# Kernel optimization log

Hardware: AMD Instinct MI355X
Metric: run time of the kernel (lower is better)

The kernel has to match this reference:

```python
import jax, jax.numpy as jnp
import numpy as np

HEADS = 8
EPS = 1e-5


def setup_inputs() -> dict:
    key = jax.random.key(0)
    ks = jax.random.split(key, 8)
    B, S, C = 2, 1024, 640
    n_refs = 4
    return {
        "hidden_states": jax.random.normal(ks[0], (B, S, C), jnp.float32),
        "ref_key": jax.random.normal(ks[1], (B, n_refs, S, C), jnp.float32),
        "ref_value": jax.random.normal(ks[2], (B, n_refs, S, C), jnp.float32),
        "Wq": jax.random.normal(ks[3], (C, C), jnp.float32) * (C ** -0.5),
        "Wk": jax.random.normal(ks[4], (C, C), jnp.float32) * (C ** -0.5),
        "Wv": jax.random.normal(ks[5], (C, C), jnp.float32) * (C ** -0.5),
        "Wo": jax.random.normal(ks[6], (C, C), jnp.float32) * (C ** -0.5),
        "bo": jnp.zeros((C,), jnp.float32),
    }


def reference(hidden_states, ref_key, ref_value, Wq, Wk, Wv, Wo, bo):
    B, S, C = hidden_states.shape
    H = HEADS
    D = C // H
    n = ref_key.shape[1]

    # projections (self-attention: encoder_hidden_states is None)
    q = hidden_states @ Wq
    k = hidden_states @ Wk
    v = hidden_states @ Wv

    def split_heads(x):  # [B, S, C] -> [B, H, S, D]
        return x.reshape(B, -1, H, D).transpose(0, 2, 1, 3)

    qh, kh, vh = split_heads(q), split_heads(k), split_heads(v)

    # per-reference head split: [B, n, S, C] -> [B, H, n, S, D]
    rk = ref_key.reshape(B, n, S, H, D).transpose(0, 3, 1, 2, 4)
    rv = ref_value.reshape(B, n, S, H, D).transpose(0, 3, 1, 2, 4)

    # AdaIN: style stats from value over its seq dim (unbiased std, as torch),
    # content stats per reference over that ref's seq dim.
    style_mean = vh.mean(axis=2, keepdims=True)[:, :, None]                 # [B,H,1,1,D]
    style_std = vh.std(axis=2, keepdims=True, ddof=1)[:, :, None] + EPS     # [B,H,1,1,D]
    content_mean = rv.mean(axis=3, keepdims=True)                           # [B,H,n,1,D]
    content_std = rv.std(axis=3, keepdims=True, ddof=1) + EPS               # [B,H,n,1,D]
    rv = (rv - content_mean) / content_std * style_std + style_mean

    # train_input=True: self KV first, then refs concatenated along kv axis
    k_ext = jnp.concatenate([kh, rk.reshape(B, H, n * S, D)], axis=2)  # [B,H,(1+n)S,D]
    v_ext = jnp.concatenate([vh, rv.reshape(B, H, n * S, D)], axis=2)

    scale = jnp.asarray(D, qh.dtype) ** -0.5
    scores = jnp.einsum("bhqd,bhkd->bhqk", qh, k_ext) * scale
    probs = jax.nn.softmax(scores, axis=-1)
    out = jnp.einsum("bhqk,bhkd->bhqd", probs, v_ext)

    out = out.transpose(0, 2, 1, 3).reshape(B, S, C)  # batch_to_head_dim
    return out @ Wo + bo  # to_out[0]; dropout is identity at eval
```

## Files before the change

kernel.cpp:

```cpp
#include <hip/hip_runtime.h>
#include <hip/hip_bf16.h>

typedef short short8 __attribute__((ext_vector_type(8)));
typedef short short4v __attribute__((ext_vector_type(4)));
typedef float f32x4 __attribute__((ext_vector_type(4)));

#define NB 2
#define NS 1024
#define NC 640
#define NH 8
#define ND 80
#define NRF 4
#define NL 5120
#define EPSF 1e-5f
#define QSCL 0.16129861f

__device__ __forceinline__ unsigned short f2bf(float f){
  unsigned int u = __float_as_uint(f);
  u += 0x7FFFu + ((u>>16)&1u);
  return (unsigned short)(u>>16);
}
__device__ __forceinline__ float bf2f(unsigned short s){
  return __uint_as_float(((unsigned)s)<<16);
}

__global__ void __launch_bounds__(256) k_cast_hs(const float* __restrict__ hs,
                                                 unsigned short* __restrict__ X){
  int i = (blockIdx.x*256 + threadIdx.x)*4;
  const float4 v = *(const float4*)(hs + i);
  uint2 pk;
  pk.x = (unsigned)f2bf(v.x) | ((unsigned)f2bf(v.y)<<16);
  pk.y = (unsigned)f2bf(v.z) | ((unsigned)f2bf(v.w)<<16);
  *(uint2*)(X + i) = pk;
}

__global__ void __launch_bounds__(256) k_transpose_w(const float* __restrict__ Wq,
    const float* __restrict__ Wk, const float* __restrict__ Wv, const float* __restrict__ Wo,
    unsigned short* __restrict__ WT){
  const float* W = (blockIdx.z==0)?Wq:(blockIdx.z==1)?Wk:(blockIdx.z==2)?Wv:Wo;
  unsigned short* out = WT + (size_t)blockIdx.z*NC*NC;
  int n0 = blockIdx.x*64, k0 = blockIdx.y*64;
  __shared__ unsigned short tile[64][65];
  int t = threadIdx.x;
  int cl = (t&15)*4, rl = t>>4;
  #pragma unroll
  for(int kk=0;kk<4;kk++){
    int kl = rl + kk*16;
    float4 v = *(const float4*)(W + (size_t)(k0+kl)*NC + n0 + cl);
    tile[kl][cl+0]=f2bf(v.x); tile[kl][cl+1]=f2bf(v.y);
    tile[kl][cl+2]=f2bf(v.z); tile[kl][cl+3]=f2bf(v.w);
  }
  __syncthreads();
  #pragma unroll
  for(int nn=0;nn<4;nn++){
    int nl = rl + nn*16;
    unsigned short a=tile[cl+0][nl], b=tile[cl+1][nl], c=tile[cl+2][nl], d=tile[cl+3][nl];
    uint2 pk; pk.x = (unsigned)a|((unsigned)b<<16); pk.y = (unsigned)c|((unsigned)d<<16);
    *(uint2*)(out + (size_t)(n0+nl)*NC + k0 + cl) = pk;
  }
}

__global__ void __launch_bounds__(256) k_gemm_qkv(const unsigned short* __restrict__ X,
    const unsigned short* __restrict__ WT, unsigned short* __restrict__ qbuf,
    unsigned short* __restrict__ kext, unsigned short* __restrict__ vTx){
  __shared__ unsigned short As[64*40], Bs[64*40];
  int mode = blockIdx.z;
  const unsigned short* Wt = WT + (size_t)mode*NC*NC;
  int M0 = blockIdx.x*64, N0 = blockIdx.y*64;
  int t = threadIdx.x, w = t>>6, lane = t&63, lr = lane&15, lg = lane>>4;
  int row = t>>2, seg = t&3;
  f32x4 acc[4];
  #pragma unroll
  for(int j=0;j<4;j++) acc[j] = (f32x4){0.f,0.f,0.f,0.f};
  for(int k0=0;k0<NC;k0+=32){
    uint4 a  = *(const uint4*)(X  + (size_t)(M0+row)*NC + k0 + seg*8);
    uint4 bq = *(const uint4*)(Wt + (size_t)(N0+row)*NC + k0 + seg*8);
    __syncthreads();
    *(uint4*)&As[row*40+seg*8] = a;
    *(uint4*)&Bs[row*40+seg*8] = bq;
    __syncthreads();
    short8 af = *(const short8*)&As[(w*16+lr)*40 + lg*8];
    #pragma unroll
    for(int j=0;j<4;j++){
      short8 bf = *(const short8*)&Bs[(j*16+lr)*40 + lg*8];
      acc[j] = __builtin_amdgcn_mfma_f32_16x16x32_bf16(af, bf, acc[j], 0,0,0);
    }
  }
  #pragma unroll
  for(int j=0;j<4;j++){
    int n = N0 + j*16 + lr;
    int h = n/ND, d = n - h*ND;
    #pragma unroll
    for(int r=0;r<4;r++){
      int m = M0 + w*16 + lg*4 + r;
      int b = m>>10, s = m&1023;
      float val = acc[j][r];
      if(mode==0){
        qbuf[(size_t)(((b<<3)|h)*NS + s)*ND + d] = f2bf(val*QSCL);
      } else if(mode==1){
        kext[(size_t)(((b<<3)|h)*NL + s)*ND + d] = f2bf(val);
      } else {
        vTx[(size_t)(((b<<3)|h)*ND + d)*NL + s] = f2bf(val);
      }
    }
  }
}

__global__ void __launch_bounds__(256) k_stats_self(const unsigned short* __restrict__ vTx,
    float* __restrict__ smean, float* __restrict__ sstd){
  int gw = blockIdx.x*4 + (threadIdx.x>>6);
  int lane = threadIdx.x&63;
  int b = gw/NC, c = gw%NC;
  int h = c/ND, d = c - h*ND;
  const unsigned short* row = vTx + (size_t)((b*NH + h)*ND + d)*NL;
  short8 v0 = *(const short8*)(row + lane*16);
  short8 v1 = *(const short8*)(row + lane*16 + 8);
  float sum=0.f, ss=0.f;
  #pragma unroll
  for(int j=0;j<8;j++){
    float x = bf2f((unsigned short)v0[j]); sum+=x; ss+=x*x;
    float y = bf2f((unsigned short)v1[j]); sum+=y; ss+=y*y;
  }
  #pragma unroll
  for(int m=1;m<=32;m<<=1){
    sum += __shfl_xor(sum, m);
    ss  += __shfl_xor(ss, m);
  }
  if(lane==0){
    float mean = sum*(1.f/1024.f);
    float var  = fmaxf(0.f,(ss - sum*sum*(1.f/1024.f))*(1.f/1023.f));
    smean[b*NC+c]=mean; sstd[b*NC+c]=sqrtf(var)+EPSF;
  }
}

__global__ void __launch_bounds__(256) k_stats_ref(const float* __restrict__ ref_value,
    float* __restrict__ cmean, float* __restrict__ cstd){
  int bid = blockIdx.x;
  int cg = bid%10, src = (bid/10)&3, b = bid/40;
  int t = threadIdx.x, cl = t&63, sg = t>>6;
  int c = cg*64 + cl;
  const float* base = ref_value + (size_t)(b*NRF + src)*NS*NC + c;
  float sum=0.f, ss=0.f;
  for(int i=0;i<256;i++){
    float x = base[(size_t)(sg*256+i)*NC];
    sum += x; ss += x*x;
  }
  __shared__ float r0[4][64], r1[4][64];
  r0[sg][cl]=sum; r1[sg][cl]=ss;
  __syncthreads();
  if(t<64){
    float S=0.f,Q=0.f;
    #pragma unroll
    for(int gg=0;gg<4;gg++){S+=r0[gg][t];Q+=r1[gg][t];}
    float mean = S*(1.f/1024.f);
    float var  = fmaxf(0.f,(Q - S*S*(1.f/1024.f))*(1.f/1023.f));
    int cc = cg*64+t;
    cmean[(b*NRF+src)*NC+cc]=mean;
    cstd[(b*NRF+src)*NC+cc]=sqrtf(var)+EPSF;
  }
}

__global__ void __launch_bounds__(256) k_scalebias(const float* __restrict__ smean,
    const float* __restrict__ sstd, const float* __restrict__ cmean, const float* __restrict__ cstd,
    float* __restrict__ scl, float* __restrict__ bia){
  int g = blockIdx.x*256+threadIdx.x;
  int c = g%NC; int b = g/(NRF*NC);
  float sc = sstd[b*NC+c]/cstd[g];
  bia[g] = smean[b*NC+c] - cmean[g]*sc;
  scl[g] = sc;
}

__global__ void __launch_bounds__(256) k_pack_k(const float* __restrict__ ref_key,
                                                unsigned short* __restrict__ kext){
  int g = blockIdx.x*256+threadIdx.x;
  size_t e = (size_t)g*4;
  int c = (int)(e%NC); int s = (int)((e/NC)&1023); int r = (int)((e/(NC*NS))&3); int b = (int)(e/((size_t)NC*NS*NRF));
  float4 v = *(const float4*)(ref_key + e);
  int h = c/ND, d = c - h*ND;
  uint2 pk;
  pk.x = (unsigned)f2bf(v.x)|((unsigned)f2bf(v.y)<<16);
  pk.y = (unsigned)f2bf(v.z)|((unsigned)f2bf(v.w)<<16);
  *(uint2*)(kext + (size_t)(((b<<3)|h)*NL + NS + r*NS + s)*ND + d) = pk;
}

__global__ void __launch_bounds__(256) k_pack_v(const float* __restrict__ ref_value,
    const float* __restrict__ scl, const float* __restrict__ bia, unsigned short* __restrict__ vTx){
  int bid=blockIdx.x;
  int ct=bid%10, st=(bid/10)&15, r=(bid/160)&3, b=bid/640;
  int c0=ct*64, s0=st*64;
  __shared__ float tile[64][68];
  int t=threadIdx.x;
  int cl=(t&15)*4, rl=t>>4;
  #pragma unroll
  for(int ss=0;ss<4;ss++){
    int srow = rl+ss*16;
    float4 v = *(const float4*)(ref_value + (size_t)((b*NRF+r)*NS + s0+srow)*NC + c0+cl);
    tile[srow][cl+0]=v.x; tile[srow][cl+1]=v.y; tile[srow][cl+2]=v.z; tile[srow][cl+3]=v.w;
  }
  __syncthreads();
  #pragma unroll
  for(int cc=0;cc<4;cc++){
    int crow = rl+cc*16;
    int c = c0+crow;
    float sc = scl[(b*NRF+r)*NC+c], bi = bia[(b*NRF+r)*NC+c];
    int h=c/ND, d=c-h*ND;
    unsigned short o0=f2bf(tile[(t&15)*4+0][crow]*sc+bi);
    unsigned short o1=f2bf(tile[(t&15)*4+1][crow]*sc+bi);
    unsigned short o2=f2bf(tile[(t&15)*4+2][crow]*sc+bi);
    unsigned short o3=f2bf(tile[(t&15)*4+3][crow]*sc+bi);
    uint2 pk; pk.x=(unsigned)o0|((unsigned)o1<<16); pk.y=(unsigned)o2|((unsigned)o3<<16);
    *(uint2*)(vTx + (size_t)(((b<<3)|h)*ND + d)*NL + NS + r*NS + s0 + (t&15)*4) = pk;
  }
}

__global__ void __launch_bounds__(256) k_attn(const unsigned short* __restrict__ qbuf,
    const unsigned short* __restrict__ kext, const unsigned short* __restrict__ vTx,
    float* __restrict__ pacc0, float* __restrict__ pacc1, float* __restrict__ pml){
  __shared__ unsigned short Ks[64*88];
  __shared__ unsigned short Vs[80*88];

  int p = blockIdx.x;
  int logical = (p&7)*64 + (p>>3);
  int tile = logical>>1;
  int part = logical&1;
  int bh = tile>>4, qti = tile&15;
  int t = threadIdx.x, w = t>>6, lane = t&63, lr = lane&15, lg = lane>>4;

  const unsigned short* kb = kext + (size_t)bh*NL*ND;
  const unsigned short* vb = vTx  + (size_t)bh*ND*NL;

  const unsigned short* qrow = qbuf + (size_t)(bh*NS + qti*64 + w*16 + lr)*ND;
  short8 qf0 = *(const short8*)(qrow + lg*8);
  short8 qf1 = *(const short8*)(qrow + 32 + lg*8);
  short4v q4 = *(const short4v*)(qrow + 64 + lg*4);
  short8 qft = {q4[0],q4[1],q4[2],q4[3],(short)0,(short)0,(short)0,(short)0};

  int rowA = t/10,       segA = t - 10*(t/10);
  int rowB = (t+256)/10, segB = (t+256) - 10*((t+256)/10);
  int rowC = (t+512)/10, segC = (t+512) - 10*((t+512)/10);
  int vd = t>>3, vs = t&7;

  f32x4 acc[5];
  #pragma unroll
  for(int dt=0;dt<5;dt++) acc[dt] = (f32x4){0.f,0.f,0.f,0.f};
  float mrun = -1e30f, lrun = 0.f;

  for(int i=0;i<40;i++){
    int key0 = (part*40 + i)*64;
    uint4 ra  = *(const uint4*)(kb + (size_t)(key0+rowA)*ND + segA*8);
    uint4 rb  = *(const uint4*)(kb + (size_t)(key0+rowB)*ND + segB*8);
    uint4 rc; if(t<128) rc = *(const uint4*)(kb + (size_t)(key0+rowC)*ND + segC*8);
    uint4 rv0 = *(const uint4*)(vb + (size_t)vd*NL + key0 + vs*8);
    uint4 rv1 = *(const uint4*)(vb + (size_t)(vd+32)*NL + key0 + vs*8);
    uint4 rv2; if(t<128) rv2 = *(const uint4*)(vb + (size_t)(vd+64)*NL + key0 + vs*8);
    __syncthreads();
    *(uint4*)&Ks[rowA*88 + segA*8] = ra;
    *(uint4*)&Ks[rowB*88 + segB*8] = rb;
    if(t<128) *(uint4*)&Ks[rowC*88 + segC*8] = rc;
    *(uint4*)&Vs[vd*88 + vs*8] = rv0;
    *(uint4*)&Vs[(vd+32)*88 + vs*8] = rv1;
    if(t<128) *(uint4*)&Vs[(vd+64)*88 + vs*8] = rv2;
    __syncthreads();

    f32x4 sc[4];
    #pragma unroll
    for(int mt=0;mt<4;mt++){
      const unsigned short* kr = &Ks[(mt*16+lr)*88];
      short8 kf0 = *(const short8*)(kr + lg*8);
      short8 kf1 = *(const short8*)(kr + 32 + lg*8);
      short4v k4 = *(const short4v*)(kr + 64 + lg*4);
      short8 kft = {k4[0],k4[1],k4[2],k4[3],(short)0,(short)0,(short)0,(short)0};
      f32x4 s = (f32x4){0.f,0.f,0.f,0.f};
      s = __builtin_amdgcn_mfma_f32_16x16x32_bf16(kf0, qf0, s, 0,0,0);
      s = __builtin_amdgcn_mfma_f32_16x16x32_bf16(kf1, qf1, s, 0,0,0);
      s = __builtin_amdgcn_mfma_f32_16x16x32_bf16(kft, qft, s, 0,0,0);
      sc[mt] = s;
    }

    float tmax = -1e30f;
    #pragma unroll
    for(int mt=0;mt<4;mt++){
      #pragma unroll
      for(int r=0;r<4;r++) tmax = fmaxf(tmax, sc[mt][r]);
    }
    tmax = fmaxf(tmax, __shfl_xor(tmax,16));
    tmax = fmaxf(tmax, __shfl_xor(tmax,32));
    float mnew = fmaxf(mrun, tmax);
    float corr = exp2f(mrun - mnew);
    float pvv[16]; float ps = 0.f;
    #pragma unroll
    for(int mt=0;mt<4;mt++){
      #pragma unroll
      for(int r=0;r<4;r++){ float e = exp2f(sc[mt][r]-mnew); pvv[mt*4+r]=e; ps+=e; }
    }
    ps += __shfl_xor(ps,16);
    ps += __shfl_xor(ps,32);
    lrun = lrun*corr + ps;
    mrun = mnew;
    #pragma unroll
    for(int dt=0;dt<5;dt++) acc[dt] *= corr;

    short8 pb[2];
    #pragma unroll
    for(int u=0;u<2;u++){
      #pragma unroll
      for(int j=0;j<4;j++){
        pb[u][j]   = (short)f2bf(pvv[u*8+j]);
        pb[u][4+j] = (short)f2bf(pvv[u*8+4+j]);
      }
    }
    #pragma unroll
    for(int u=0;u<2;u++){
      #pragma unroll
      for(int dt=0;dt<5;dt++){
        const unsigned short* vr = &Vs[(dt*16+lr)*88 + u*32 + lg*4];
        short4v v0 = *(const short4v*)(vr);
        short4v v1 = *(const short4v*)(vr + 16);
        short8 vf = {v0[0],v0[1],v0[2],v0[3],v1[0],v1[1],v1[2],v1[3]};
        acc[dt] = __builtin_amdgcn_mfma_f32_16x16x32_bf16(vf, pb[u], acc[dt], 0,0,0);
      }
    }
  }

  float* pa = (part ? pacc1 : pacc0) + (size_t)tile*5120;
  int q = w*16 + lr;
  #pragma unroll
  for(int dt=0;dt<5;dt++){
    *(f32x4*)(pa + q*80 + dt*16 + lg*4) = acc[dt];
  }
  if(lg==0){
    pml[(size_t)logical*128 + q*2 + 0] = mrun;
    pml[(size_t)logical*128 + q*2 + 1] = lrun;
  }
}

__global__ void __launch_bounds__(256) k_combine(const float* __restrict__ pacc0,
    const float* __restrict__ pacc1, const float* __restrict__ pml,
    unsigned short* __restrict__ attnO){
  int tile = blockIdx.x;
  int bh = tile>>4, qti = tile&15;
  int b = bh>>3, h = bh&7;
  int t = threadIdx.x;
  #pragma unroll
  for(int j=0;j<5;j++){
    int e = (t + j*256)*4;
    int q = e/80, d = e - (e/80)*80;
    float m0 = pml[(size_t)(tile*2+0)*128 + q*2], l0 = pml[(size_t)(tile*2+0)*128 + q*2 + 1];
    float m1 = pml[(size_t)(tile*2+1)*128 + q*2], l1 = pml[(size_t)(tile*2+1)*128 + q*2 + 1];
    float mm = fmaxf(m0,m1);
    float c0 = exp2f(m0-mm), c1 = exp2f(m1-mm);
    float inv = 1.f/(l0*c0 + l1*c1);
    c0 *= inv; c1 *= inv;
    float4 a0 = *(const float4*)(pacc0 + (size_t)tile*5120 + e);
    float4 a1 = *(const float4*)(pacc1 + (size_t)tile*5120 + e);
    uint2 pk;
    pk.x = (unsigned)f2bf(a0.x*c0+a1.x*c1) | ((unsigned)f2bf(a0.y*c0+a1.y*c1)<<16);
    pk.y = (unsigned)f2bf(a0.z*c0+a1.z*c1) | ((unsigned)f2bf(a0.w*c0+a1.w*c1)<<16);
    *(uint2*)(attnO + (size_t)(b*NS + qti*64 + q)*NC + h*ND + d) = pk;
  }
}

__global__ void __launch_bounds__(256) k_gemm_out(const unsigned short* __restrict__ A,
    const unsigned short* __restrict__ WT, const float* __restrict__ bo, float* __restrict__ out){
  __shared__ unsigned short As[64*40], Bs[64*40];
  const unsigned short* Wt = WT + (size_t)3*NC*NC;
  int M0 = blockIdx.x*64, N0 = blockIdx.y*64;
  int t = threadIdx.x, w = t>>6, lane = t&63, lr = lane&15, lg = lane>>4;
  int row = t>>2, seg = t&3;
  f32x4 acc[4];
  #pragma unroll
  for(int j=0;j<4;j++) acc[j] = (f32x4){0.f,0.f,0.f,0.f};
  for(int k0=0;k0<NC;k0+=32){
    uint4 a  = *(const uint4*)(A  + (size_t)(M0+row)*NC + k0 + seg*8);
    uint4 bq = *(const uint4*)(Wt + (size_t)(N0+row)*NC + k0 + seg*8);
    __syncthreads();
    *(uint4*)&As[row*40+seg*8] = a;
    *(uint4*)&Bs[row*40+seg*8] = bq;
    __syncthreads();
    short8 af = *(const short8*)&As[(w*16+lr)*40 + lg*8];
    #pragma unroll
    for(int j=0;j<4;j++){
      short8 bf = *(const short8*)&Bs[(j*16+lr)*40 + lg*8];
      acc[j] = __builtin_amdgcn_mfma_f32_16x16x32_bf16(af, bf, acc[j], 0,0,0);
    }
  }
  #pragma unroll
  for(int j=0;j<4;j++){
    int n = N0 + j*16 + lr;
    float bb = bo[n];
    #pragma unroll
    for(int r=0;r<4;r++){
      int m = M0 + w*16 + lg*4 + r;
      out[(size_t)m*NC + n] = acc[j][r] + bb;
    }
  }
}

extern "C" void kernel_launch(void* const* d_in, const int* in_sizes, int n_in,
                              void* d_out, int out_size, void* d_ws, size_t ws_size,
                              hipStream_t stream) {
  const float* hs        = (const float*)d_in[0];
  const float* ref_key   = (const float*)d_in[1];
  const float* ref_value = (const float*)d_in[2];
  const float* Wq = (const float*)d_in[3];
  const float* Wk = (const float*)d_in[4];
  const float* Wv = (const float*)d_in[5];
  const float* Wo = (const float*)d_in[6];
  const float* bo = (const float*)d_in[7];
  float* out = (float*)d_out;

  char* ws = (char*)d_ws;
  size_t off = 0;
  auto alloc = [&](size_t bytes)->char*{
    char* p = ws + off;
    off += (bytes + 255) & ~(size_t)255;
    return p;
  };
  unsigned short* X    = (unsigned short*)alloc((size_t)NB*NS*NC*2);
  unsigned short* WT   = (unsigned short*)alloc((size_t)4*NC*NC*2);
  unsigned short* qbuf = (unsigned short*)alloc((size_t)NB*NH*NS*ND*2);
  unsigned short* kext = (unsigned short*)alloc((size_t)NB*NH*NL*ND*2);
  unsigned short* vTx  = (unsigned short*)alloc((size_t)NB*NH*ND*NL*2);
  float* pacc1 = (float*)alloc((size_t)256*5120*4);
  float* pml   = (float*)alloc((size_t)512*128*4);
  float* smean = (float*)alloc((size_t)NB*NC*4);
  float* sstd  = (float*)alloc((size_t)NB*NC*4);
  float* cmean = (float*)alloc((size_t)NB*NRF*NC*4);
  float* cstd  = (float*)alloc((size_t)NB*NRF*NC*4);
  float* scl   = (float*)alloc((size_t)NB*NRF*NC*4);
  float* bia   = (float*)alloc((size_t)NB*NRF*NC*4);
  unsigned short* attn = X;
  float* pacc0 = out;

  k_cast_hs<<<1280, 256, 0, stream>>>(hs, X);
  k_transpose_w<<<dim3(10,10,4), 256, 0, stream>>>(Wq, Wk, Wv, Wo, WT);
  k_gemm_qkv<<<dim3(32,10,3), 256, 0, stream>>>(X, WT, qbuf, kext, vTx);
  k_pack_k<<<5120, 256, 0, stream>>>(ref_key, kext);
  k_stats_self<<<320, 256, 0, stream>>>(vTx, smean, sstd);
  k_stats_ref<<<80, 256, 0, stream>>>(ref_value, cmean, cstd);
  k_scalebias<<<20, 256, 0, stream>>>(smean, sstd, cmean, cstd, scl, bia);
  k_pack_v<<<1280, 256, 0, stream>>>(ref_value, scl, bia, vTx);
  k_attn<<<512, 256, 0, stream>>>(qbuf, kext, vTx, pacc0, pacc1, pml);
  k_combine<<<256, 256, 0, stream>>>(pacc0, pacc1, pml, attn);
  k_gemm_out<<<dim3(32,10), 256, 0, stream>>>(attn, WT, bo, out);
}
```

Measured before the change: 237.4 us.

## Split attention KV into four parts, lazy softmax rescale, fold scale/bias into pack_v

Attention blocks now split the 5120-key range into four partitions instead of two, launching 1024 blocks with four partial accumulators merged in the combine kernel. This gives more parallelism across CUs for the 512 prior blocks. The online softmax skips the max update and the accumulator rescale when no score exceeds the running max by more than 8, which removes per-tile correction work. The separate scale/bias kernel is removed and its math is inlined into k_pack_v, saving a launch. In exchange, combine reads more partial buffers and more workspace is used.

```diff
diff --git a/kernel.cpp b/kernel.cpp
--- a/kernel.cpp
+++ b/kernel.cpp
@@ -160,16 +160,6 @@
   }
 }
 
-__global__ void __launch_bounds__(256) k_scalebias(const float* __restrict__ smean,
-    const float* __restrict__ sstd, const float* __restrict__ cmean, const float* __restrict__ cstd,
-    float* __restrict__ scl, float* __restrict__ bia){
-  int g = blockIdx.x*256+threadIdx.x;
-  int c = g%NC; int b = g/(NRF*NC);
-  float sc = sstd[b*NC+c]/cstd[g];
-  bia[g] = smean[b*NC+c] - cmean[g]*sc;
-  scl[g] = sc;
-}
-
 __global__ void __launch_bounds__(256) k_pack_k(const float* __restrict__ ref_key,
                                                 unsigned short* __restrict__ kext){
   int g = blockIdx.x*256+threadIdx.x;
@@ -184,7 +174,9 @@
 }
 
 __global__ void __launch_bounds__(256) k_pack_v(const float* __restrict__ ref_value,
-    const float* __restrict__ scl, const float* __restrict__ bia, unsigned short* __restrict__ vTx){
+    const float* __restrict__ smean, const float* __restrict__ sstd,
+    const float* __restrict__ cmean, const float* __restrict__ cstd,
+    unsigned short* __restrict__ vTx){
   int bid=blockIdx.x;
   int ct=bid%10, st=(bid/10)&15, r=(bid/160)&3, b=bid/640;
   int c0=ct*64, s0=st*64;
@@ -202,7 +194,8 @@
   for(int cc=0;cc<4;cc++){
     int crow = rl+cc*16;
     int c = c0+crow;
-    float sc = scl[(b*NRF+r)*NC+c], bi = bia[(b*NRF+r)*NC+c];
+    float sc = sstd[b*NC+c]/cstd[(b*NRF+r)*NC+c];
+    float bi = smean[b*NC+c] - cmean[(b*NRF+r)*NC+c]*sc;
     int h=c/ND, d=c-h*ND;
     unsigned short o0=f2bf(tile[(t&15)*4+0][crow]*sc+bi);
     unsigned short o1=f2bf(tile[(t&15)*4+1][crow]*sc+bi);
@@ -215,14 +208,15 @@
 
 __global__ void __launch_bounds__(256) k_attn(const unsigned short* __restrict__ qbuf,
     const unsigned short* __restrict__ kext, const unsigned short* __restrict__ vTx,
-    float* __restrict__ pacc0, float* __restrict__ pacc1, float* __restrict__ pml){
+    float* __restrict__ pacc0, float* __restrict__ pacc1,
+    float* __restrict__ pacc2, float* __restrict__ pacc3, float* __restrict__ pml){
   __shared__ unsigned short Ks[64*88];
   __shared__ unsigned short Vs[80*88];
 
   int p = blockIdx.x;
-  int logical = (p&7)*64 + (p>>3);
-  int tile = logical>>1;
-  int part = logical&1;
+  int logical = (p&7)*128 + (p>>3);
+  int tile = logical>>2;
+  int part = logical&3;
   int bh = tile>>4, qti = tile&15;
   int t = threadIdx.x, w = t>>6, lane = t&63, lr = lane&15, lg = lane>>4;
 
@@ -245,8 +239,8 @@
   for(int dt=0;dt<5;dt++) acc[dt] = (f32x4){0.f,0.f,0.f,0.f};
   float mrun = -1e30f, lrun = 0.f;
 
-  for(int i=0;i<40;i++){
-    int key0 = (part*40 + i)*64;
+  for(int i=0;i<20;i++){
+    int key0 = (part*20 + i)*64;
     uint4 ra  = *(const uint4*)(kb + (size_t)(key0+rowA)*ND + segA*8);
     uint4 rb  = *(const uint4*)(kb + (size_t)(key0+rowB)*ND + segB*8);
     uint4 rc; if(t<128) rc = *(const uint4*)(kb + (size_t)(key0+rowC)*ND + segC*8);
@@ -285,20 +279,34 @@
     }
     tmax = fmaxf(tmax, __shfl_xor(tmax,16));
     tmax = fmaxf(tmax, __shfl_xor(tmax,32));
-    float mnew = fmaxf(mrun, tmax);
-    float corr = exp2f(mrun - mnew);
-    float pvv[16]; float ps = 0.f;
-    #pragma unroll
-    for(int mt=0;mt<4;mt++){
-      #pragma unroll
-      for(int r=0;r<4;r++){ float e = exp2f(sc[mt][r]-mnew); pvv[mt*4+r]=e; ps+=e; }
-    }
-    ps += __shfl_xor(ps,16);
-    ps += __shfl_xor(ps,32);
-    lrun = lrun*corr + ps;
-    mrun = mnew;
-    #pragma unroll
-    for(int dt=0;dt<5;dt++) acc[dt] *= corr;
+
+    float pvv[16];
+    if(__all(tmax <= mrun + 8.0f)){
+      float ps = 0.f;
+      #pragma unroll
+      for(int mt=0;mt<4;mt++){
+        #pragma unroll
+        for(int r=0;r<4;r++){ float e = exp2f(sc[mt][r]-mrun); pvv[mt*4+r]=e; ps+=e; }
+      }
+      ps += __shfl_xor(ps,16);
+      ps += __shfl_xor(ps,32);
+      lrun += ps;
+    } else {
+      float mnew = fmaxf(mrun, tmax);
+      float corr = exp2f(mrun - mnew);
+      float ps = 0.f;
+      #pragma unroll
+      for(int mt=0;mt<4;mt++){
+        #pragma unroll
+        for(int r=0;r<4;r++){ float e = exp2f(sc[mt][r]-mnew); pvv[mt*4+r]=e; ps+=e; }
+      }
+      ps += __shfl_xor(ps,16);
+      ps += __shfl_xor(ps,32);
+      lrun = lrun*corr + ps;
+      mrun = mnew;
+      #pragma unroll
+      for(int dt=0;dt<5;dt++) acc[dt] *= corr;
+    }
 
     short8 pb[2];
     #pragma unroll
@@ -322,7 +330,7 @@
     }
   }
 
-  float* pa = (part ? pacc1 : pacc0) + (size_t)tile*5120;
+  float* pa = (part==0?pacc0:part==1?pacc1:part==2?pacc2:pacc3) + (size_t)tile*5120;
   int q = w*16 + lr;
   #pragma unroll
   for(int dt=0;dt<5;dt++){
@@ -335,7 +343,8 @@
 }
 
 __global__ void __launch_bounds__(256) k_combine(const float* __restrict__ pacc0,
-    const float* __restrict__ pacc1, const float* __restrict__ pml,
+    const float* __restrict__ pacc1, const float* __restrict__ pacc2,
+    const float* __restrict__ pacc3, const float* __restrict__ pml,
     unsigned short* __restrict__ attnO){
   int tile = blockIdx.x;
   int bh = tile>>4, qti = tile&15;
@@ -345,17 +354,23 @@
   for(int j=0;j<5;j++){
     int e = (t + j*256)*4;
     int q = e/80, d = e - (e/80)*80;
-    float m0 = pml[(size_t)(tile*2+0)*128 + q*2], l0 = pml[(size_t)(tile*2+0)*128 + q*2 + 1];
-    float m1 = pml[(size_t)(tile*2+1)*128 + q*2], l1 = pml[(size_t)(tile*2+1)*128 + q*2 + 1];
-    float mm = fmaxf(m0,m1);
-    float c0 = exp2f(m0-mm), c1 = exp2f(m1-mm);
-    float inv = 1.f/(l0*c0 + l1*c1);
-    c0 *= inv; c1 *= inv;
+    float m0 = pml[(size_t)(tile*4+0)*128 + q*2], l0 = pml[(size_t)(tile*4+0)*128 + q*2 + 1];
+    float m1 = pml[(size_t)(tile*4+1)*128 + q*2], l1 = pml[(size_t)(tile*4+1)*128 + q*2 + 1];
+    float m2 = pml[(size_t)(tile*4+2)*128 + q*2], l2 = pml[(size_t)(tile*4+2)*128 + q*2 + 1];
+    float m3 = pml[(size_t)(tile*4+3)*128 + q*2], l3 = pml[(size_t)(tile*4+3)*128 + q*2 + 1];
+    float mm = fmaxf(fmaxf(m0,m1), fmaxf(m2,m3));
+    float c0 = exp2f(m0-mm), c1 = exp2f(m1-mm), c2 = exp2f(m2-mm), c3 = exp2f(m3-mm);
+    float inv = 1.f/(l0*c0 + l1*c1 + l2*c2 + l3*c3);
+    c0 *= inv; c1 *= inv; c2 *= inv; c3 *= inv;
     float4 a0 = *(const float4*)(pacc0 + (size_t)tile*5120 + e);
     float4 a1 = *(const float4*)(pacc1 + (size_t)tile*5120 + e);
+    float4 a2 = *(const float4*)(pacc2 + (size_t)tile*5120 + e);
+    float4 a3 = *(const float4*)(pacc3 + (size_t)tile*5120 + e);
     uint2 pk;
-    pk.x = (unsigned)f2bf(a0.x*c0+a1.x*c1) | ((unsigned)f2bf(a0.y*c0+a1.y*c1)<<16);
-    pk.y = (unsigned)f2bf(a0.z*c0+a1.z*c1) | ((unsigned)f2bf(a0.w*c0+a1.w*c1)<<16);
+    pk.x = (unsigned)f2bf(a0.x*c0+a1.x*c1+a2.x*c2+a3.x*c3)
+         | ((unsigned)f2bf(a0.y*c0+a1.y*c1+a2.y*c2+a3.y*c3)<<16);
+    pk.y = (unsigned)f2bf(a0.z*c0+a1.z*c1+a2.z*c2+a3.z*c3)
+         | ((unsigned)f2bf(a0.w*c0+a1.w*c1+a2.w*c2+a3.w*c3)<<16);
     *(uint2*)(attnO + (size_t)(b*NS + qti*64 + q)*NC + h*ND + d) = pk;
   }
 }
@@ -422,13 +437,13 @@
   unsigned short* kext = (unsigned short*)alloc((size_t)NB*NH*NL*ND*2);
   unsigned short* vTx  = (unsigned short*)alloc((size_t)NB*NH*ND*NL*2);
   float* pacc1 = (float*)alloc((size_t)256*5120*4);
-  float* pml   = (float*)alloc((size_t)512*128*4);
+  float* pacc2 = (float*)alloc((size_t)256*5120*4);
+  float* pacc3 = (float*)alloc((size_t)256*5120*4);
+  float* pml   = (float*)alloc((size_t)1024*128*4);
   float* smean = (float*)alloc((size_t)NB*NC*4);
   float* sstd  = (float*)alloc((size_t)NB*NC*4);
   float* cmean = (float*)alloc((size_t)NB*NRF*NC*4);
   float* cstd  = (float*)alloc((size_t)NB*NRF*NC*4);
-  float* scl   = (float*)alloc((size_t)NB*NRF*NC*4);
-  float* bia   = (float*)alloc((size_t)NB*NRF*NC*4);
   unsigned short* attn = X;
   float* pacc0 = out;
 
@@ -438,9 +453,8 @@
   k_pack_k<<<5120, 256, 0, stream>>>(ref_key, kext);
   k_stats_self<<<320, 256, 0, stream>>>(vTx, smean, sstd);
   k_stats_ref<<<80, 256, 0, stream>>>(ref_value, cmean, cstd);
-  k_scalebias<<<20, 256, 0, stream>>>(smean, sstd, cmean, cstd, scl, bia);
-  k_pack_v<<<1280, 256, 0, stream>>>(ref_value, scl, bia, vTx);
-  k_attn<<<512, 256, 0, stream>>>(qbuf, kext, vTx, pacc0, pacc1, pml);
-  k_combine<<<256, 256, 0, stream>>>(pacc0, pacc1, pml, attn);
+  k_pack_v<<<1280, 256, 0, stream>>>(ref_value, smean, sstd, cmean, cstd, vTx);
+  k_attn<<<1024, 256, 0, stream>>>(qbuf, kext, vTx, pacc0, pacc1, pacc2, pacc3, pml);
+  k_combine<<<256, 256, 0, stream>>>(pacc0, pacc1, pacc2, pacc3, pml, attn);
   k_gemm_out<<<dim3(32,10), 256, 0, stream>>>(attn, WT, bo, out);
 }
```

Result: faster. 229.7 us (-3.2%).
